# Optimization experiments

Measured on AMD Instinct MI355X. Metric: run time of the kernel, lower is better.

The kernel has to match this reference:

```python
import jax, jax.numpy as jnp
import numpy as np

N, E, DIM, H = 50000, 800000, 64, 2
HD = H * DIM


def setup_inputs() -> dict:
    key = jax.random.key(0)
    ks = jax.random.split(key, 16)
    s = 0.05
    return {
        "x": jax.random.normal(ks[0], (N, DIM), jnp.float32),
        "edge_index": jax.random.randint(ks[1], (2, E), 0, N, jnp.int64),
        "Wq": jax.random.normal(ks[2], (DIM, HD), jnp.float32) * s,
        "bq": jax.random.normal(ks[3], (HD,), jnp.float32) * s,
        "Wk": jax.random.normal(ks[4], (DIM, HD), jnp.float32) * s,
        "bk": jax.random.normal(ks[5], (HD,), jnp.float32) * s,
        "Wv": jax.random.normal(ks[6], (DIM, HD), jnp.float32) * s,
        "bv": jax.random.normal(ks[7], (HD,), jnp.float32) * s,
        "Wskip": jax.random.normal(ks[8], (DIM, HD), jnp.float32) * s,
        "bskip": jax.random.normal(ks[9], (HD,), jnp.float32) * s,
        "Wc": jax.random.normal(ks[10], (HD, DIM), jnp.float32) * s,
        "bc": jax.random.normal(ks[11], (DIM,), jnp.float32) * s,
        "gamma": jnp.ones((DIM,), jnp.float32),
        "beta": jnp.zeros((DIM,), jnp.float32),
    }


def reference(x, edge_index, Wq, bq, Wk, bk, Wv, bv, Wskip, bskip, Wc, bc, gamma, beta):
    src, dst = edge_index[0], edge_index[1]  # messages flow src -> dst
    # TransformerConv: per-head q/k/v projections, [N, H, D]
    q = (x @ Wq + bq).reshape(N, H, DIM)
    k = (x @ Wk + bk).reshape(N, H, DIM)
    v = (x @ Wv + bv).reshape(N, H, DIM)
    scale = 1.0 / np.sqrt(DIM).astype(np.float32)
    # edge-wise attention logits: [E, H]
    alpha = jnp.einsum('ehd,ehd->eh', q[dst], k[src]) * scale
    # segment softmax over incoming edges of each dst node (PyG softmax)
    amax = jax.ops.segment_max(alpha, dst, num_segments=N)
    a = jnp.exp(alpha - amax[dst])
    asum = jax.ops.segment_sum(a, dst, num_segments=N)
    a = a / (asum[dst] + 1e-16)
    # weighted scatter-aggregate of values: [N, H, D] -> concat heads
    out = jax.ops.segment_sum(a[:, :, None] * v[src], dst, num_segments=N)
    out = out.reshape(N, HD)
    # root/skip connection (root_weight=True default)
    out = out + (x @ Wskip + bskip)
    # concat linear: H*D -> dim
    out = out @ Wc + bc
    # pyg.LayerNorm default mode='graph': normalize over ALL nodes+features
    out = out - out.mean()
    out = out / (out.std() + 1e-5)  # std with unbiased=False (jnp default ddof=0)
    return out * gamma + beta
```

## Files before the change

kernel.cpp:

```cpp
#include <hip/hip_runtime.h>
#include <hip/hip_bf16.h>

#define N_NODES 50000
#define N_EDGES 800000
#define DIM 64
#define NHEAD 2
#define HD 128
#define NCOL 448
#define MAXDEG 64

#define NBIN 196
#define BCAP 6144
#define ACH 2048
#define BIN_BLKS 391

#define PREP_B 112
#define PROJ_B 782
#define ATTN_B 3125

#define QSCALE 0.18033688011112042f

typedef short bf16x8 __attribute__((ext_vector_type(8)));
typedef float f32x16 __attribute__((ext_vector_type(16)));
typedef float f32x2 __attribute__((ext_vector_type(2)));

__device__ __forceinline__ unsigned short f2bf(float f) {
    unsigned u = __float_as_uint(f);
    unsigned r = (u + 0x7fffu + ((u >> 16) & 1u)) >> 16;
    return (unsigned short)r;
}
__device__ __forceinline__ unsigned char f2fp8(float f) {
    int r = __builtin_amdgcn_cvt_pk_fp8_f32(f, f, 0, false);
    return (unsigned char)(r & 0xff);
}

__global__ __launch_bounds__(256) void k_pb(
    const int* __restrict__ ei,
    const float* __restrict__ Wq, const float* __restrict__ bq,
    const float* __restrict__ Wk, const float* __restrict__ bk,
    const float* __restrict__ Wv, const float* __restrict__ bv,
    const float* __restrict__ Wskip, const float* __restrict__ bskip,
    const float* __restrict__ Wc, const float* __restrict__ bc,
    unsigned short* __restrict__ WallT, float* __restrict__ ball,
    int* __restrict__ bincnt, unsigned* __restrict__ bins,
    double* __restrict__ sacc)
{
    const int t = threadIdx.x;
    if (blockIdx.x < PREP_B) {
        if (blockIdx.x == 0) { sacc[t] = 0.0; sacc[256 + t] = 0.0; }
        int gid = blockIdx.x * 256 + t;
        const int j = gid >> 6;
        const int d = gid & 63;
        float w, bb;
        if (j < 128) {
            w = Wq[d * HD + j] * QSCALE;
            bb = bq[j] * QSCALE;
        } else if (j < 256) {
            int jj = j - 128;
            w = Wk[d * HD + jj];
            bb = bk[jj];
        } else if (j < 384) {
            int jj = j - 256;
            int h = jj >> 6, jc = jj & 63;
            float s = 0.f, sb = 0.f;
            for (int c = 0; c < 64; c++) {
                float wc = Wc[(h * 64 + c) * DIM + jc];
                s  += Wv[d * HD + h * 64 + c] * wc;
                sb += bv[h * 64 + c] * wc;
            }
            w = s; bb = sb;
        } else {
            int jj = j - 384;
            float s = 0.f, sb = bc[jj];
            for (int c = 0; c < HD; c++) {
                float wc = Wc[c * DIM + jj];
                s  += Wskip[d * HD + c] * wc;
                sb += bskip[c] * wc;
            }
            w = s; bb = sb;
        }
        WallT[gid] = f2bf(w);
        if (d == 0) ball[j] = bb;
        return;
    }
    __shared__ int hist[256];
    __shared__ int gbase[256];
    const int e0 = (blockIdx.x - PREP_B) * ACH;
    hist[t] = 0;
    __syncthreads();
    unsigned pk8[8];
    int bin8[8], sl8[8];
#pragma unroll
    for (int k = 0; k < 8; k++) {
        int e = e0 + t + k * 256;
        if (e < N_EDGES) {
            int src = ei[e];
            int d = ei[N_EDGES + e];
            int bin = d >> 8;
            pk8[k] = (unsigned)(((d & 255) << 16) | src);
            bin8[k] = bin;
            sl8[k] = atomicAdd(&hist[bin], 1);
        } else {
            bin8[k] = -1;
        }
    }
    __syncthreads();
    if (t < NBIN) {
        int h = hist[t];
        if (h > 0) gbase[t] = atomicAdd(&bincnt[t], h);
    }
    __syncthreads();
#pragma unroll
    for (int k = 0; k < 8; k++) {
        int bin = bin8[k];
        if (bin >= 0) {
            int pos = gbase[bin] + sl8[k];
            if (pos < BCAP) bins[(size_t)bin * BCAP + pos] = pk8[k];
        }
    }
}

__global__ __launch_bounds__(256) void k_ep(
    const float* __restrict__ x,
    const unsigned short* __restrict__ WallT, const float* __restrict__ ball,
    float* __restrict__ q, unsigned char* __restrict__ kv, float* __restrict__ skipc,
    const int* __restrict__ bincnt, const unsigned* __restrict__ bins,
    int* __restrict__ deg, unsigned short* __restrict__ elist)
{
    __shared__ __align__(16) unsigned char smem[65536];
    const int blk = blockIdx.x;
    const int t = threadIdx.x;
    if (blk >= PROJ_B) {
        const int bin = blk - PROJ_B;
        int* nodecnt = (int*)smem;
        nodecnt[t] = 0;
        __syncthreads();
        int cnt = bincnt[bin]; if (cnt > BCAP) cnt = BCAP;
        const unsigned* bp = bins + (size_t)bin * BCAP;
        for (int i = t; i < cnt; i += 256) {
            unsigned p = bp[i];
            int local = p >> 16;
            int src = p & 0xffff;
            int sl = atomicAdd(&nodecnt[local], 1);
            if (sl < MAXDEG)
                elist[((size_t)((bin << 8) | local)) * MAXDEG + sl] = (unsigned short)src;
        }
        __syncthreads();
        int node = (bin << 8) + t;
        if (node < N_NODES) {
            int dgv = nodecnt[t];
            deg[node] = dgv > MAXDEG ? MAXDEG : dgv;
        }
        return;
    }
    float* q_s = (float*)smem;
    unsigned char* kv_s = smem + 32768;
    float* sk_s = (float*)(smem + 49152);

    const int w = t >> 6;
    const int lane = t & 63;
    const int col = lane & 31;
    const int khalf = lane >> 5;
    const int nloc0 = (w >> 1) * 32;
    const int n0 = blk * 64 + nloc0;
    const int ct0 = (w & 1) * 7;
    const int rowbase = 4 * khalf;

    int nread = n0 + col; if (nread >= N_NODES) nread = N_NODES - 1;
    const float* ap = x + (size_t)nread * 64 + khalf * 8;
    bf16x8 afrag[4];
#pragma unroll
    for (int kk = 0; kk < 4; kk++) {
        float4 xa = *((const float4*)(ap + kk * 16));
        float4 xb4 = *((const float4*)(ap + kk * 16 + 4));
        bf16x8 f;
        f[0] = (short)f2bf(xa.x); f[1] = (short)f2bf(xa.y);
        f[2] = (short)f2bf(xa.z); f[3] = (short)f2bf(xa.w);
        f[4] = (short)f2bf(xb4.x); f[5] = (short)f2bf(xb4.y);
        f[6] = (short)f2bf(xb4.z); f[7] = (short)f2bf(xb4.w);
        afrag[kk] = f;
    }

    for (int tt = 0; tt < 7; tt++) {
        const int gc = (ct0 + tt) * 32 + col;
        const float b = ball[gc];
        f32x16 acc;
#pragma unroll
        for (int r = 0; r < 16; r++) acc[r] = b;
        const unsigned short* bp = WallT + (size_t)gc * 64 + khalf * 8;
#pragma unroll
        for (int kk = 0; kk < 4; kk++) {
            bf16x8 bfrag = *((const bf16x8*)(bp + kk * 16));
            acc = __builtin_amdgcn_mfma_f32_32x32x16_bf16(afrag[kk], bfrag, acc, 0, 0, 0);
        }
        if (gc < 128) {
#pragma unroll
            for (int r = 0; r < 16; r++) {
                int nl = nloc0 + rowbase + (r & 3) + 8 * (r >> 2);
                q_s[nl * 128 + gc] = acc[r];
            }
        } else if (gc < 384) {
            int ch = gc - 128;
            int half = ch >> 7;
            int cc = ch & 127;
            int h = cc >> 6, c = cc & 63;
            int pos = half * 128 + ((c >> 3) << 4) + (h << 3) + (c & 7);
#pragma unroll
            for (int r = 0; r < 16; r++) {
                int nl = nloc0 + rowbase + (r & 3) + 8 * (r >> 2);
                kv_s[nl * 256 + pos] = f2fp8(acc[r]);
            }
        } else {
            int c = gc - 384;
#pragma unroll
            for (int r = 0; r < 16; r++) {
                int nl = nloc0 + rowbase + (r & 3) + 8 * (r >> 2);
                sk_s[nl * 64 + c] = acc[r];
            }
        }
    }
    __syncthreads();
    const size_t nbase = (size_t)blk * 64;
    const int nrem = (int)(N_NODES - nbase);
    {
        const float4* s4 = (const float4*)q_s;
        float4* g4 = (float4*)(q + nbase * HD);
        int lim = nrem >= 64 ? 2048 : nrem * 32;
#pragma unroll
        for (int kk = 0; kk < 8; kk++) {
            int i = t + kk * 256;
            if (i < lim) g4[i] = s4[i];
        }
    }
    {
        const uint4* s4 = (const uint4*)kv_s;
        uint4* g4 = (uint4*)(kv + nbase * 256);
        int lim = nrem >= 64 ? 1024 : nrem * 16;
#pragma unroll
        for (int kk = 0; kk < 4; kk++) {
            int i = t + kk * 256;
            if (i < lim) g4[i] = s4[i];
        }
    }
    {
        const float4* s4 = (const float4*)sk_s;
        float4* g4 = (float4*)(skipc + nbase * DIM);
        int lim = nrem >= 64 ? 1024 : nrem * 16;
#pragma unroll
        for (int kk = 0; kk < 4; kk++) {
            int i = t + kk * 256;
            if (i < lim) g4[i] = s4[i];
        }
    }
}

__global__ __launch_bounds__(256) void k_attn(
    const float* __restrict__ q, const unsigned char* __restrict__ kv,
    const float* __restrict__ skipc,
    const int* __restrict__ deg, const unsigned short* __restrict__ elist,
    float* __restrict__ out, double* __restrict__ sacc)
{
    const int w = threadIdx.x >> 6;
    const int lane = threadIdx.x & 63;
    const int e = (lane >> 3) & 1;
    const int j = lane & 7;
    const int n = blockIdx.x * 16 + w * 4 + (lane >> 4);
    const bool nvalid = n < N_NODES;
    const int nn = nvalid ? n : N_NODES - 1;

    const uint2 E = *((const uint2*)(elist + (size_t)nn * MAXDEG + (lane & 15) * 4));
    int dg = nvalid ? deg[nn] : 0;
    if (dg > MAXDEG) dg = MAXDEG;
    int dgmax = dg;
    {
        int o1 = __shfl_xor(dgmax, 16, 64); if (o1 > dgmax) dgmax = o1;
        int o2 = __shfl_xor(dgmax, 32, 64); if (o2 > dgmax) dgmax = o2;
    }

    const float4* qp4 = (const float4*)(q + (size_t)nn * HD);
    const float4 qa = qp4[2 * j],      qb = qp4[2 * j + 1];
    const float4 qc = qp4[16 + 2 * j], qd = qp4[17 + 2 * j];
    f32x2 q0[4], q1[4];
    q0[0] = (f32x2){qa.x, qa.y}; q0[1] = (f32x2){qa.z, qa.w};
    q0[2] = (f32x2){qb.x, qb.y}; q0[3] = (f32x2){qb.z, qb.w};
    q1[0] = (f32x2){qc.x, qc.y}; q1[1] = (f32x2){qc.z, qc.w};
    q1[2] = (f32x2){qd.x, qd.y}; q1[3] = (f32x2){qd.z, qd.w};

    f32x2 acc0[4], acc1[4];
#pragma unroll
    for (int i = 0; i < 4; i++) {
        acc0[i] = (f32x2){0.f, 0.f};
        acc1[i] = (f32x2){0.f, 0.f};
    }
    float l0 = 0.f, l1 = 0.f;

    for (int b = 0; b < dgmax; b += 2) {
        const int k = b + e;
        const bool valid = k < dg;
        unsigned dwd = ((b >> 1) & 1) ? E.y : E.x;
        int sd = __shfl((int)dwd, (lane & 48) | (b >> 2), 64);
        unsigned v16 = e ? (((unsigned)sd) >> 16) : (((unsigned)sd) & 0xffffu);
        int s = valid ? (int)v16 : 0;
        const uint4* kp = (const uint4*)(kv + (size_t)s * 256);
        const uint4 K = kp[j];
        const uint4 V = kp[8 + j];
        f32x2 p0v = q0[0] * __builtin_amdgcn_cvt_pk_f32_fp8(K.x, false);
        p0v += q0[1] * __builtin_amdgcn_cvt_pk_f32_fp8(K.x, true);
        p0v += q0[2] * __builtin_amdgcn_cvt_pk_f32_fp8(K.y, false);
        p0v += q0[3] * __builtin_amdgcn_cvt_pk_f32_fp8(K.y, true);
        f32x2 p1v = q1[0] * __builtin_amdgcn_cvt_pk_f32_fp8(K.z, false);
        p1v += q1[1] * __builtin_amdgcn_cvt_pk_f32_fp8(K.z, true);
        p1v += q1[2] * __builtin_amdgcn_cvt_pk_f32_fp8(K.w, false);
        p1v += q1[3] * __builtin_amdgcn_cvt_pk_f32_fp8(K.w, true);
        float p0 = p0v[0] + p0v[1];
        float p1 = p1v[0] + p1v[1];
#pragma unroll
        for (int off = 1; off < 8; off <<= 1) {
            p0 += __shfl_xor(p0, off, 64);
            p1 += __shfl_xor(p1, off, 64);
        }
        float w0 = valid ? __builtin_amdgcn_exp2f(p0) : 0.f;
        float w1 = valid ? __builtin_amdgcn_exp2f(p1) : 0.f;
        l0 += w0; l1 += w1;
        f32x2 w0v = {w0, w0}, w1v = {w1, w1};
        acc0[0] += w0v * __builtin_amdgcn_cvt_pk_f32_fp8(V.x, false);
        acc0[1] += w0v * __builtin_amdgcn_cvt_pk_f32_fp8(V.x, true);
        acc0[2] += w0v * __builtin_amdgcn_cvt_pk_f32_fp8(V.y, false);
        acc0[3] += w0v * __builtin_amdgcn_cvt_pk_f32_fp8(V.y, true);
        acc1[0] += w1v * __builtin_amdgcn_cvt_pk_f32_fp8(V.z, false);
        acc1[1] += w1v * __builtin_amdgcn_cvt_pk_f32_fp8(V.z, true);
        acc1[2] += w1v * __builtin_amdgcn_cvt_pk_f32_fp8(V.w, false);
        acc1[3] += w1v * __builtin_amdgcn_cvt_pk_f32_fp8(V.w, true);
    }

    l0 += __shfl_xor(l0, 8, 64);
    l1 += __shfl_xor(l1, 8, 64);
    float* a0 = (float*)acc0;
    float* a1 = (float*)acc1;
#pragma unroll
    for (int i = 0; i < 8; i++) {
        a0[i] += __shfl_xor(a0[i], 8, 64);
        a1[i] += __shfl_xor(a1[i], 8, 64);
    }

    const float inv0 = 1.f / (l0 + 1e-16f), inv1 = 1.f / (l1 + 1e-16f);
    const float4 sk4 = ((const float4*)(skipc + (size_t)nn * DIM))[2 * j + e];
    const int cb = e * 4;
    float o0 = a0[cb + 0] * inv0 + a1[cb + 0] * inv1 + sk4.x;
    float o1 = a0[cb + 1] * inv0 + a1[cb + 1] * inv1 + sk4.y;
    float o2 = a0[cb + 2] * inv0 + a1[cb + 2] * inv1 + sk4.z;
    float o3 = a0[cb + 3] * inv0 + a1[cb + 3] * inv1 + sk4.w;
    if (nvalid) {
        float4 r = {o0, o1, o2, o3};
        ((float4*)(out + (size_t)n * DIM))[2 * j + e] = r;
    }
    float s_ = 0.f, ss = 0.f;
    if (nvalid) {
        s_ = o0 + o1 + o2 + o3;
        ss = o0 * o0 + o1 * o1 + o2 * o2 + o3 * o3;
    }
#pragma unroll
    for (int off = 1; off < 64; off <<= 1) {
        s_ += __shfl_xor(s_, off, 64);
        ss += __shfl_xor(ss, off, 64);
    }
    if (lane == 0) {
        int slot = (blockIdx.x * 4 + w) & 255;
        atomicAdd(&sacc[slot], (double)s_);
        atomicAdd(&sacc[256 + slot], (double)ss);
    }
}

__global__ __launch_bounds__(256) void k_norm(
    float* __restrict__ out, const double* __restrict__ sacc,
    const float* __restrict__ gamma, const float* __restrict__ beta)
{
    const int t = threadIdx.x;
    __shared__ double red[8];
    double s = sacc[t];
    double ss = sacc[256 + t];
#pragma unroll
    for (int off = 32; off > 0; off >>= 1) {
        s  += __shfl_down(s, off);
        ss += __shfl_down(ss, off);
    }
    int wv = t >> 6;
    if ((t & 63) == 0) { red[wv * 2] = s; red[wv * 2 + 1] = ss; }
    __syncthreads();
    double S  = red[0] + red[2] + red[4] + red[6];
    double SS = red[1] + red[3] + red[5] + red[7];
    const double cnt = (double)N_NODES * (double)DIM;
    double mean = S / cnt;
    double var  = SS / cnt - mean * mean;
    if (var < 0.0) var = 0.0;
    float mf = (float)mean;
    float inv = 1.0f / ((float)sqrt(var) + 1e-5f);
    int i = blockIdx.x * 256 + t;
    if (i >= N_NODES * DIM / 4) return;
    float4 v = ((const float4*)out)[i];
    float4 gv = ((const float4*)gamma)[i & 15];
    float4 bv2 = ((const float4*)beta)[i & 15];
    v.x = (v.x - mf) * inv * gv.x + bv2.x;
    v.y = (v.y - mf) * inv * gv.y + bv2.y;
    v.z = (v.z - mf) * inv * gv.z + bv2.z;
    v.w = (v.w - mf) * inv * gv.w + bv2.w;
    ((float4*)out)[i] = v;
}

extern "C" void kernel_launch(void* const* d_in, const int* in_sizes, int n_in,
                              void* d_out, int out_size, void* d_ws, size_t ws_size,
                              hipStream_t stream) {
    const float* x     = (const float*)d_in[0];
    const int*   ei    = (const int*)d_in[1];
    const float* Wq    = (const float*)d_in[2];
    const float* bq    = (const float*)d_in[3];
    const float* Wk    = (const float*)d_in[4];
    const float* bk    = (const float*)d_in[5];
    const float* Wv    = (const float*)d_in[6];
    const float* bv    = (const float*)d_in[7];
    const float* Wsk   = (const float*)d_in[8];
    const float* bsk   = (const float*)d_in[9];
    const float* Wc    = (const float*)d_in[10];
    const float* bc    = (const float*)d_in[11];
    const float* gamma = (const float*)d_in[12];
    const float* beta  = (const float*)d_in[13];
    float* out = (float*)d_out;

    double* sacc = (double*)d_ws;
    float* ws = (float*)(sacc + 512);
    const size_t NF = (size_t)N_NODES * HD;
    float* q = ws;
    unsigned char* kv = (unsigned char*)(ws + NF);
    float* skipc = (float*)(kv + (size_t)N_NODES * 256);
    unsigned short* WallT = (unsigned short*)(skipc + (size_t)N_NODES * DIM);
    float* ball   = (float*)(WallT + NCOL * 64);
    int* bincnt   = (int*)(ball + NCOL);
    unsigned* bins = (unsigned*)(bincnt + 256);
    int* deg      = (int*)(bins + (size_t)NBIN * BCAP);
    unsigned short* elist = (unsigned short*)(deg + N_NODES);

    hipMemsetAsync(bincnt, 0, 256 * sizeof(int), stream);
    hipLaunchKernelGGL(k_pb, dim3(PREP_B + BIN_BLKS), dim3(256), 0, stream,
                       ei, Wq, bq, Wk, bk, Wv, bv, Wsk, bsk, Wc, bc,
                       WallT, ball, bincnt, bins, sacc);
    hipLaunchKernelGGL(k_ep, dim3(PROJ_B + NBIN), dim3(256), 0, stream,
                       x, WallT, ball, q, kv, skipc, bincnt, bins, deg, elist);
    hipLaunchKernelGGL(k_attn, dim3(ATTN_B), dim3(256), 0, stream,
                       q, kv, skipc, deg, elist, out, sacc);
    hipLaunchKernelGGL(k_norm, dim3(N_NODES * DIM / 4 / 256 + 1), dim3(256), 0, stream,
                       out, sacc, gamma, beta);
}
```

Before: 172.9 us.

## Store q in bf16 and software-prefetch next K/V row in attention loop

The projection kernel now writes q as bf16 instead of fp32. This halves q's global write and read traffic and shrinks its shared-memory staging buffer, which allows a smaller LDS allocation. The attention kernel unpacks q from bf16. Its edge loop is also restructured to issue the gather of the next edge pair's K/V row before computing on the current one, so memory latency overlaps with compute. The cost is extra registers for the prefetched row and some loss of precision in q.

Measured after the change: 174.2 us. No clear change (+0.7%).

```diff
diff --git a/kernel.cpp b/kernel.cpp
--- a/kernel.cpp
+++ b/kernel.cpp
@@ -32,6 +32,12 @@
 __device__ __forceinline__ unsigned char f2fp8(float f) {
     int r = __builtin_amdgcn_cvt_pk_fp8_f32(f, f, 0, false);
     return (unsigned char)(r & 0xff);
+}
+__device__ __forceinline__ f32x2 bf2x2(unsigned v) {
+    f32x2 r;
+    r[0] = __uint_as_float(v << 16);
+    r[1] = __uint_as_float(v & 0xffff0000u);
+    return r;
 }
 
 __global__ __launch_bounds__(256) void k_pb(
@@ -123,11 +129,12 @@
 __global__ __launch_bounds__(256) void k_ep(
     const float* __restrict__ x,
     const unsigned short* __restrict__ WallT, const float* __restrict__ ball,
-    float* __restrict__ q, unsigned char* __restrict__ kv, float* __restrict__ skipc,
+    unsigned short* __restrict__ q, unsigned char* __restrict__ kv,
+    float* __restrict__ skipc,
     const int* __restrict__ bincnt, const unsigned* __restrict__ bins,
     int* __restrict__ deg, unsigned short* __restrict__ elist)
 {
-    __shared__ __align__(16) unsigned char smem[65536];
+    __shared__ __align__(16) unsigned char smem[49152];
     const int blk = blockIdx.x;
     const int t = threadIdx.x;
     if (blk >= PROJ_B) {
@@ -153,9 +160,9 @@
         }
         return;
     }
-    float* q_s = (float*)smem;
-    unsigned char* kv_s = smem + 32768;
-    float* sk_s = (float*)(smem + 49152);
+    unsigned short* q_s = (unsigned short*)smem;
+    unsigned char* kv_s = smem + 16384;
+    float* sk_s = (float*)(smem + 32768);
 
     const int w = t >> 6;
     const int lane = t & 63;
@@ -197,7 +204,7 @@
 #pragma unroll
             for (int r = 0; r < 16; r++) {
                 int nl = nloc0 + rowbase + (r & 3) + 8 * (r >> 2);
-                q_s[nl * 128 + gc] = acc[r];
+                q_s[nl * 128 + gc] = f2bf(acc[r]);
             }
         } else if (gc < 384) {
             int ch = gc - 128;
@@ -223,11 +230,11 @@
     const size_t nbase = (size_t)blk * 64;
     const int nrem = (int)(N_NODES - nbase);
     {
-        const float4* s4 = (const float4*)q_s;
-        float4* g4 = (float4*)(q + nbase * HD);
-        int lim = nrem >= 64 ? 2048 : nrem * 32;
-#pragma unroll
-        for (int kk = 0; kk < 8; kk++) {
+        const uint4* s4 = (const uint4*)q_s;
+        uint4* g4 = (uint4*)(q + nbase * HD);
+        int lim = nrem >= 64 ? 1024 : nrem * 16;
+#pragma unroll
+        for (int kk = 0; kk < 4; kk++) {
             int i = t + kk * 256;
             if (i < lim) g4[i] = s4[i];
         }
@@ -255,7 +262,7 @@
 }
 
 __global__ __launch_bounds__(256) void k_attn(
-    const float* __restrict__ q, const unsigned char* __restrict__ kv,
+    const unsigned short* __restrict__ q, const unsigned char* __restrict__ kv,
     const float* __restrict__ skipc,
     const int* __restrict__ deg, const unsigned short* __restrict__ elist,
     float* __restrict__ out, double* __restrict__ sacc)
@@ -277,14 +284,11 @@
         int o2 = __shfl_xor(dgmax, 32, 64); if (o2 > dgmax) dgmax = o2;
     }
 
-    const float4* qp4 = (const float4*)(q + (size_t)nn * HD);
-    const float4 qa = qp4[2 * j],      qb = qp4[2 * j + 1];
-    const float4 qc = qp4[16 + 2 * j], qd = qp4[17 + 2 * j];
+    const uint4* qp4 = (const uint4*)(q + (size_t)nn * HD);
+    const uint4 Qa = qp4[j], Qb = qp4[8 + j];
     f32x2 q0[4], q1[4];
-    q0[0] = (f32x2){qa.x, qa.y}; q0[1] = (f32x2){qa.z, qa.w};
-    q0[2] = (f32x2){qb.x, qb.y}; q0[3] = (f32x2){qb.z, qb.w};
-    q1[0] = (f32x2){qc.x, qc.y}; q1[1] = (f32x2){qc.z, qc.w};
-    q1[2] = (f32x2){qd.x, qd.y}; q1[3] = (f32x2){qd.z, qd.w};
+    q0[0] = bf2x2(Qa.x); q0[1] = bf2x2(Qa.y); q0[2] = bf2x2(Qa.z); q0[3] = bf2x2(Qa.w);
+    q1[0] = bf2x2(Qb.x); q1[1] = bf2x2(Qb.y); q1[2] = bf2x2(Qb.z); q1[3] = bf2x2(Qb.w);
 
     f32x2 acc0[4], acc1[4];
 #pragma unroll
@@ -294,43 +298,54 @@
     }
     float l0 = 0.f, l1 = 0.f;
 
-    for (int b = 0; b < dgmax; b += 2) {
-        const int k = b + e;
-        const bool valid = k < dg;
-        unsigned dwd = ((b >> 1) & 1) ? E.y : E.x;
-        int sd = __shfl((int)dwd, (lane & 48) | (b >> 2), 64);
-        unsigned v16 = e ? (((unsigned)sd) >> 16) : (((unsigned)sd) & 0xffffu);
-        int s = valid ? (int)v16 : 0;
-        const uint4* kp = (const uint4*)(kv + (size_t)s * 256);
-        const uint4 K = kp[j];
-        const uint4 V = kp[8 + j];
-        f32x2 p0v = q0[0] * __builtin_amdgcn_cvt_pk_f32_fp8(K.x, false);
-        p0v += q0[1] * __builtin_amdgcn_cvt_pk_f32_fp8(K.x, true);
-        p0v += q0[2] * __builtin_amdgcn_cvt_pk_f32_fp8(K.y, false);
-        p0v += q0[3] * __builtin_amdgcn_cvt_pk_f32_fp8(K.y, true);
-        f32x2 p1v = q1[0] * __builtin_amdgcn_cvt_pk_f32_fp8(K.z, false);
-        p1v += q1[1] * __builtin_amdgcn_cvt_pk_f32_fp8(K.z, true);
-        p1v += q1[2] * __builtin_amdgcn_cvt_pk_f32_fp8(K.w, false);
-        p1v += q1[3] * __builtin_amdgcn_cvt_pk_f32_fp8(K.w, true);
-        float p0 = p0v[0] + p0v[1];
-        float p1 = p1v[0] + p1v[1];
-#pragma unroll
-        for (int off = 1; off < 8; off <<= 1) {
-            p0 += __shfl_xor(p0, off, 64);
-            p1 += __shfl_xor(p1, off, 64);
-        }
-        float w0 = valid ? __builtin_amdgcn_exp2f(p0) : 0.f;
-        float w1 = valid ? __builtin_amdgcn_exp2f(p1) : 0.f;
-        l0 += w0; l1 += w1;
-        f32x2 w0v = {w0, w0}, w1v = {w1, w1};
-        acc0[0] += w0v * __builtin_amdgcn_cvt_pk_f32_fp8(V.x, false);
-        acc0[1] += w0v * __builtin_amdgcn_cvt_pk_f32_fp8(V.x, true);
-        acc0[2] += w0v * __builtin_amdgcn_cvt_pk_f32_fp8(V.y, false);
-        acc0[3] += w0v * __builtin_amdgcn_cvt_pk_f32_fp8(V.y, true);
-        acc1[0] += w1v * __builtin_amdgcn_cvt_pk_f32_fp8(V.z, false);
-        acc1[1] += w1v * __builtin_amdgcn_cvt_pk_f32_fp8(V.z, true);
-        acc1[2] += w1v * __builtin_amdgcn_cvt_pk_f32_fp8(V.w, false);
-        acc1[3] += w1v * __builtin_amdgcn_cvt_pk_f32_fp8(V.w, true);
+    if (dgmax > 0) {
+        int sd0 = __shfl((int)E.x, (lane & 48), 64);
+        unsigned v0 = e ? (((unsigned)sd0) >> 16) : (((unsigned)sd0) & 0xffffu);
+        int s0 = (e < dg) ? (int)v0 : 0;
+        const uint4* kp0 = (const uint4*)(kv + (size_t)s0 * 256);
+        uint4 K = kp0[j], V = kp0[8 + j];
+
+        for (int b = 0; b < dgmax; b += 2) {
+            uint4 Kn = {0, 0, 0, 0}, Vn = {0, 0, 0, 0};
+            const int bn = b + 2;
+            if (bn < dgmax) {
+                unsigned dwd = ((bn >> 1) & 1) ? E.y : E.x;
+                int sd = __shfl((int)dwd, (lane & 48) | (bn >> 2), 64);
+                unsigned v16 = e ? (((unsigned)sd) >> 16) : (((unsigned)sd) & 0xffffu);
+                int sn = ((bn + e) < dg) ? (int)v16 : 0;
+                const uint4* kpn = (const uint4*)(kv + (size_t)sn * 256);
+                Kn = kpn[j]; Vn = kpn[8 + j];
+            }
+            const bool valid = (b + e) < dg;
+            f32x2 p0v = q0[0] * __builtin_amdgcn_cvt_pk_f32_fp8(K.x, false);
+            p0v += q0[1] * __builtin_amdgcn_cvt_pk_f32_fp8(K.x, true);
+            p0v += q0[2] * __builtin_amdgcn_cvt_pk_f32_fp8(K.y, false);
+            p0v += q0[3] * __builtin_amdgcn_cvt_pk_f32_fp8(K.y, true);
+            f32x2 p1v = q1[0] * __builtin_amdgcn_cvt_pk_f32_fp8(K.z, false);
+            p1v += q1[1] * __builtin_amdgcn_cvt_pk_f32_fp8(K.z, true);
+            p1v += q1[2] * __builtin_amdgcn_cvt_pk_f32_fp8(K.w, false);
+            p1v += q1[3] * __builtin_amdgcn_cvt_pk_f32_fp8(K.w, true);
+            float p0 = p0v[0] + p0v[1];
+            float p1 = p1v[0] + p1v[1];
+#pragma unroll
+            for (int off = 1; off < 8; off <<= 1) {
+                p0 += __shfl_xor(p0, off, 64);
+                p1 += __shfl_xor(p1, off, 64);
+            }
+            float w0 = valid ? __builtin_amdgcn_exp2f(p0) : 0.f;
+            float w1 = valid ? __builtin_amdgcn_exp2f(p1) : 0.f;
+            l0 += w0; l1 += w1;
+            f32x2 w0v = {w0, w0}, w1v = {w1, w1};
+            acc0[0] += w0v * __builtin_amdgcn_cvt_pk_f32_fp8(V.x, false);
+            acc0[1] += w0v * __builtin_amdgcn_cvt_pk_f32_fp8(V.x, true);
+            acc0[2] += w0v * __builtin_amdgcn_cvt_pk_f32_fp8(V.y, false);
+            acc0[3] += w0v * __builtin_amdgcn_cvt_pk_f32_fp8(V.y, true);
+            acc1[0] += w1v * __builtin_amdgcn_cvt_pk_f32_fp8(V.z, false);
+            acc1[1] += w1v * __builtin_amdgcn_cvt_pk_f32_fp8(V.z, true);
+            acc1[2] += w1v * __builtin_amdgcn_cvt_pk_f32_fp8(V.w, false);
+            acc1[3] += w1v * __builtin_amdgcn_cvt_pk_f32_fp8(V.w, true);
+            K = Kn; V = Vn;
+        }
     }
 
     l0 += __shfl_xor(l0, 8, 64);
@@ -427,10 +442,8 @@
     float* out = (float*)d_out;
 
     double* sacc = (double*)d_ws;
-    float* ws = (float*)(sacc + 512);
-    const size_t NF = (size_t)N_NODES * HD;
-    float* q = ws;
-    unsigned char* kv = (unsigned char*)(ws + NF);
+    unsigned short* q = (unsigned short*)(sacc + 512);
+    unsigned char* kv = (unsigned char*)(q + (size_t)N_NODES * HD);
     float* skipc = (float*)(kv + (size_t)N_NODES * 256);
     unsigned short* WallT = (unsigned short*)(skipc + (size_t)N_NODES * DIM);
     float* ball   = (float*)(WallT + NCOL * 64);
```
